# Kernel optimization log

Hardware: AMD Instinct MI355X
Metric: run time of the kernel (lower is better)

The kernel has to match this reference:

```python
import jax, jax.numpy as jnp
import numpy as np

N_EMBD = 1024
HEAD_SIZE = 64
B, T = 4, 4096


def setup_inputs() -> dict:
    key = jax.random.key(0)
    kx, kk, kq, kv = jax.random.split(key, 4)
    s = 1.0 / np.sqrt(N_EMBD)
    return {
        "x": jax.random.normal(kx, (B, T, N_EMBD), dtype=jnp.float32),
        "Wk": jax.random.normal(kk, (N_EMBD, HEAD_SIZE), dtype=jnp.float32) * s,
        "Wq": jax.random.normal(kq, (N_EMBD, HEAD_SIZE), dtype=jnp.float32) * s,
        "Wv": jax.random.normal(kv, (N_EMBD, HEAD_SIZE), dtype=jnp.float32) * s,
    }


def reference(x, Wk, Wq, Wv):
    Bb, Tt, C = x.shape
    k = x @ Wk  # [B,T,H]
    q = x @ Wq
    v = x @ Wv
    # scores scaled by C**-0.5 where C = n_embd (as in the original module)
    w = jnp.einsum('bth,bsh->bts', q, k) * (C ** -0.5)  # [B,T,T]
    causal = jnp.tril(jnp.ones((Tt, Tt), dtype=bool))
    w = jnp.where(causal, w, -jnp.inf)
    w = jax.nn.softmax(w, axis=-1)
    # dropout prob is 0.0 (eval) -> identity
    out = jnp.einsum('bts,bsh->bth', w, v)  # [B,T,H]
    return out
```

## Files before the change

### kernel.cpp

```cpp
#include <hip/hip_runtime.h>


#define BSZ 4
#define TSZ 4096
#define CSZ 1024
#define MSZ (BSZ * TSZ)
#define QT 128
#define NQT (TSZ / QT)
#define CPB 272
#define MAXC 16

typedef _Float16 half8 __attribute__((ext_vector_type(8)));
typedef _Float16 half4 __attribute__((ext_vector_type(4)));
typedef float f32x4 __attribute__((ext_vector_type(4)));

#define MFMA(a, b, c) __builtin_amdgcn_mfma_f32_16x16x32_f16((a), (b), (c), 0, 0, 0)
#define QSCALE 0.04508422002778011f

__device__ __forceinline__ int kimg(int r, int h) {
    return r * 64 + (((h >> 3) ^ (r & 7)) << 3) + (h & 7);
}
__device__ __forceinline__ int vimg(int kk, int h) {
    int p = (kk & 15) * 4 + (kk >> 4);
    return h * 64 + (((p >> 3) ^ (h & 7)) << 3) + (p & 7);
}

__device__ __forceinline__ void glds16(const _Float16* g, _Float16* l) {
    __builtin_amdgcn_global_load_lds(
        (const __attribute__((address_space(1))) void*)g,
        (__attribute__((address_space(3))) void*)l, 16, 0, 0);
}

__global__ __launch_bounds__(192) void wconv(const float* __restrict__ Wk,
                                             const float* __restrict__ Wq,
                                             const float* __restrict__ Wv,
                                             _Float16* __restrict__ Wt) {
    int k = blockIdx.x;
    int n = threadIdx.x;
    int g = k >> 6, c = (k >> 3) & 7, j = k & 7;
    const float* W = (n < 64) ? Wk : ((n < 128) ? Wq : Wv);
    float v = W[k * 64 + (n & 63)];
    if (n >= 64 && n < 128) v *= QSCALE;
    Wt[(size_t)n * 1024 + g * 64 + ((c ^ (n & 7)) << 3) + j] = (_Float16)v;
}

__global__ __launch_bounds__(512) void qkv_proj(
    const float* __restrict__ x, const _Float16* __restrict__ Wt,
    _Float16* __restrict__ qbf, _Float16* __restrict__ kvs) {
    __shared__ _Float16 wt[2][192 * 64];
    __shared__ _Float16 xt[2][64 * 64];

    int tid = threadIdx.x;
    int wave = tid >> 6, lane = tid & 63;
    int quad = lane >> 4, l16 = lane & 15;
    int row0 = blockIdx.x * 64;
    int mh = wave >> 2;
    int ctb = (wave & 3) * 3;

    f32x4 acc[6];
#pragma unroll
    for (int i = 0; i < 6; i++) acc[i] = (f32x4){0.f, 0.f, 0.f, 0.f};

    int sr = tid >> 3, sc = tid & 7;
    const float* xrow = x + (size_t)(row0 + sr) * CSZ + sc * 8;
    f32x4 p0 = *(const f32x4*)xrow;
    f32x4 p1 = *(const f32x4*)(xrow + 4);

#pragma unroll
    for (int i = 0; i < 3; i++) {
        int g = i * 512 + tid;
        glds16(Wt + ((size_t)(g >> 3)) * 1024 + (g & 7) * 8,
               &wt[0][(size_t)g * 8]);
    }

    int cur = 0;
    for (int kc = 0; kc < CSZ; kc += 64, cur ^= 1) {
        {
            _Float16 tmp[8] __attribute__((aligned(16)));
#pragma unroll
            for (int i = 0; i < 4; i++) {
                tmp[i] = (_Float16)p0[i];
                tmp[4 + i] = (_Float16)p1[i];
            }
            *(half8*)&xt[cur][sr * 64 + ((sc ^ (sr & 7)) << 3)] = *(half8*)tmp;
        }
        __syncthreads();

        if (kc + 64 < CSZ) {
#pragma unroll
            for (int i = 0; i < 3; i++) {
                int g = i * 512 + tid;
                glds16(Wt + ((size_t)(g >> 3)) * 1024 + (kc + 64) + (g & 7) * 8,
                       &wt[cur ^ 1][(size_t)g * 8]);
            }
            p0 = *(const f32x4*)(xrow + kc + 64);
            p1 = *(const f32x4*)(xrow + kc + 68);
        }

#pragma unroll
        for (int ss = 0; ss < 2; ss++) {
            half8 a0 = *(half8*)&xt[cur][(mh * 32 + l16) * 64 +
                                         (((ss * 4 + quad) ^ (l16 & 7)) << 3)];
            half8 a1 = *(half8*)&xt[cur][(mh * 32 + 16 + l16) * 64 +
                                         (((ss * 4 + quad) ^ (l16 & 7)) << 3)];
#pragma unroll
            for (int j = 0; j < 3; j++) {
                int ct = ctb + j;
                half8 bb = *(half8*)&wt[cur][(ct * 16 + l16) * 64 +
                                             (((ss * 4 + quad) ^ (l16 & 7))
                                              << 3)];
                acc[j * 2 + 0] = MFMA(a0, bb, acc[j * 2 + 0]);
                acc[j * 2 + 1] = MFMA(a1, bb, acc[j * 2 + 1]);
            }
        }
    }

#pragma unroll
    for (int j = 0; j < 3; j++) {
        int ct = ctb + j;
        int kind = ct >> 2;
        int col = (ct & 3) * 16 + l16;
#pragma unroll
        for (int m = 0; m < 2; m++) {
#pragma unroll
            for (int r = 0; r < 4; r++) {
                int row = row0 + mh * 32 + m * 16 + quad * 4 + r;
                _Float16 val = (_Float16)acc[j * 2 + m][r];
                if (kind == 0) {
                    kvs[((size_t)(row >> 6)) * 8192 + kimg(row & 63, col)] = val;
                } else if (kind == 1) {
                    qbf[(size_t)row * 64 + col] = val;
                } else {
                    kvs[((size_t)(row >> 6)) * 8192 + 4096 +
                        vimg(row & 63, col)] = val;
                }
            }
        }
    }
}

__global__ __launch_bounds__(256) void attn_partial(
    const _Float16* __restrict__ qbf, const _Float16* __restrict__ kvs,
    _Float16* __restrict__ opart, float* __restrict__ ml) {
    __shared__ _Float16 kt[2][4096];
    __shared__ _Float16 vt[2][4096];
    __shared__ _Float16 pt[QT * 64];

    int tid = threadIdx.x;
    int wave = tid >> 6, lane = tid & 63;
    int quad = lane >> 4, l16 = lane & 15;

    int id = blockIdx.x;
    int xcd = id & 7;
    int b = xcd >> 1;
    int id2 = (id >> 3) * 2 + (xcd & 1);
    int qt = 0;
    while (qt < NQT - 1 && (((qt + 2) * (qt + 2)) >> 2) <= id2) qt++;
    int chunk = id2 - (((qt + 1) * (qt + 1)) >> 2);
    int nt = 2 * (qt + 1);
    int lo = chunk * 4;
    int hi = min(lo + 4, nt);
    int part = (b * NQT + qt) * MAXC + chunk;

    const _Float16* qb = qbf + (size_t)b * TSZ * 64;
    const _Float16* kvb = kvs + (size_t)b * 64 * 8192;

    int qrow = qt * QT + wave * 32;
    half8 aq[2][2];
#pragma unroll
    for (int st = 0; st < 2; st++)
#pragma unroll
        for (int ss = 0; ss < 2; ss++)
            aq[st][ss] = *(const half8*)&qb[(size_t)(qrow + st * 16 + l16) * 64 +
                                            ss * 32 + quad * 8];

    f32x4 o[2][4];
    float l_acc[2][4];
#pragma unroll
    for (int st = 0; st < 2; st++)
#pragma unroll
        for (int ct = 0; ct < 4; ct++) {
            o[st][ct] = (f32x4){0.f, 0.f, 0.f, 0.f};
            l_acc[st][ct] = 0.f;
        }

    int soff = wave * 512 + lane * 8;

    {
        const _Float16* p0 = kvb + (size_t)lo * 8192 + soff;
        glds16(p0, &kt[0][soff]);
        glds16(p0 + 2048, &kt[0][2048 + soff]);
        glds16(p0 + 4096, &vt[0][soff]);
        glds16(p0 + 6144, &vt[0][2048 + soff]);
    }

    int cur = 0;
    for (int kti = lo; kti < hi; kti++, cur ^= 1) {
        __syncthreads();
        if (kti + 1 < hi) {
            const _Float16* p0 = kvb + (size_t)(kti + 1) * 8192 + soff;
            glds16(p0, &kt[cur ^ 1][soff]);
            glds16(p0 + 2048, &kt[cur ^ 1][2048 + soff]);
            glds16(p0 + 4096, &vt[cur ^ 1][soff]);
            glds16(p0 + 6144, &vt[cur ^ 1][2048 + soff]);
        }

        f32x4 sacc[2][4];
#pragma unroll
        for (int st = 0; st < 2; st++)
#pragma unroll
            for (int ct = 0; ct < 4; ct++)
                sacc[st][ct] = (f32x4){0.f, 0.f, 0.f, 0.f};
#pragma unroll
        for (int ss = 0; ss < 2; ss++) {
#pragma unroll
            for (int ct = 0; ct < 4; ct++) {
                half8 bb = *(half8*)&kt[cur][(ct * 16 + l16) * 64 +
                                             (((ss * 4 + quad) ^ (l16 & 7))
                                              << 3)];
                sacc[0][ct] = MFMA(aq[0][ss], bb, sacc[0][ct]);
                sacc[1][ct] = MFMA(aq[1][ss], bb, sacc[1][ct]);
            }
        }

        bool diag = (kti >= 2 * qt);
#pragma unroll
        for (int st = 0; st < 2; st++) {
#pragma unroll
            for (int r = 0; r < 4; r++) {
                int lrow = wave * 32 + st * 16 + quad * 4 + r;
                float pv[4];
#pragma unroll
                for (int ct = 0; ct < 4; ct++) {
                    float e = exp2f(sacc[st][ct][r]);
                    if (diag) {
                        int key = kti * 64 + ct * 16 + l16;
                        if (key > qt * QT + lrow) e = 0.f;
                    }
                    pv[ct] = e;
                }
                l_acc[st][r] += pv[0] + pv[1] + pv[2] + pv[3];
                half4 hp;
#pragma unroll
                for (int ct = 0; ct < 4; ct++) hp[ct] = (_Float16)pv[ct];
                int chk = (l16 >> 1) ^ (lrow & 7);
                *(half4*)&pt[lrow * 64 + chk * 8 + (l16 & 1) * 4] = hp;
            }
        }

#pragma unroll
        for (int ss = 0; ss < 2; ss++) {
            half8 ap0 = *(half8*)&pt[(wave * 32 + l16) * 64 +
                                     (((ss * 4 + quad) ^ (l16 & 7)) << 3)];
            half8 ap1 = *(half8*)&pt[(wave * 32 + 16 + l16) * 64 +
                                     (((ss * 4 + quad) ^ (l16 & 7)) << 3)];
#pragma unroll
            for (int ct = 0; ct < 4; ct++) {
                half8 bv = *(half8*)&vt[cur][(ct * 16 + l16) * 64 +
                                             (((ss * 4 + quad) ^ (l16 & 7))
                                              << 3)];
                o[0][ct] = MFMA(ap0, bv, o[0][ct]);
                o[1][ct] = MFMA(ap1, bv, o[1][ct]);
            }
        }
    }

#pragma unroll
    for (int off = 1; off < 16; off <<= 1) {
#pragma unroll
        for (int st = 0; st < 2; st++)
#pragma unroll
            for (int r = 0; r < 4; r++)
                l_acc[st][r] += __shfl_xor(l_acc[st][r], off);
    }

    _Float16* op = opart + (size_t)part * (QT * 64);
#pragma unroll
    for (int st = 0; st < 2; st++) {
#pragma unroll
        for (int r = 0; r < 4; r++) {
            int lrow = wave * 32 + st * 16 + quad * 4 + r;
            float li = l_acc[st][r];
            float inv = li > 0.f ? 1.f / li : 0.f;
#pragma unroll
            for (int ct = 0; ct < 4; ct++)
                op[lrow * 64 + ct * 16 + l16] = (_Float16)(o[st][ct][r] * inv);
            if (l16 == 0) ml[part * QT + lrow] = li;
        }
    }
}

__global__ __launch_bounds__(256) void combine(
    const _Float16* __restrict__ opart, const float* __restrict__ ml,
    float* __restrict__ out) {
    int tid = threadIdx.x;
    int row = blockIdx.x * 32 + (tid >> 3);
    int seg = (tid & 7) * 8;
    int b = row >> 12;
    int qt = (row >> 7) & (NQT - 1);
    int prow = row & (QT - 1);
    int pbase = (b * NQT + qt) * MAXC;
    int nc = (qt + 2) >> 1;

    float acc[8];
#pragma unroll
    for (int i = 0; i < 8; i++) acc[i] = 0.f;
    float lsum = 0.f;
    for (int s = 0; s < nc; s++) {
        float l = ml[(pbase + s) * QT + prow];
        lsum += l;
        half8 h = *(const half8*)&opart[(size_t)(pbase + s) * (QT * 64) +
                                        prow * 64 + seg];
#pragma unroll
        for (int i = 0; i < 8; i++) acc[i] += l * (float)h[i];
    }
    float inv = 1.f / lsum;
    float* ob = out + (size_t)row * 64 + seg;
#pragma unroll
    for (int i = 0; i < 8; i++) ob[i] = acc[i] * inv;
}

extern "C" void kernel_launch(void* const* d_in, const int* in_sizes, int n_in,
                              void* d_out, int out_size, void* d_ws,
                              size_t ws_size, hipStream_t stream) {
    (void)in_sizes; (void)n_in; (void)out_size; (void)ws_size;
    const float* x = (const float*)d_in[0];
    const float* Wk = (const float*)d_in[1];
    const float* Wq = (const float*)d_in[2];
    const float* Wv = (const float*)d_in[3];

    _Float16* Wt = (_Float16*)d_ws;
    _Float16* qbf = Wt + 192 * 1024;
    _Float16* kvs = qbf + (size_t)MSZ * 64;
    _Float16* opart = kvs + (size_t)MSZ * 128;
    float* ml = (float*)(opart + (size_t)BSZ * NQT * MAXC * QT * 64);

    wconv<<<1024, 192, 0, stream>>>(Wk, Wq, Wv, Wt);
    qkv_proj<<<MSZ / 64, 512, 0, stream>>>(x, Wt, qbf, kvs);
    attn_partial<<<BSZ * CPB, 256, 0, stream>>>(qbf, kvs, opart, ml);
    combine<<<MSZ / 32, 256, 0, stream>>>(opart, ml, (float*)d_out);
}
```

Baseline: 150.4 us.

## Use 32x32x16 MFMA with transposed S and register-resident P for PV

Rewrites the attention inner loop to compute S^T with 32x32x16 MFMAs so each lane owns one query row. P is packed to fp16 in registers and rearranged with permlane32 swaps, then fed straight into the PV MFMA, which removes the LDS round-trip through the P tile. The V storage layout changes to match, and fully masked 32-key subtiles on the diagonal are skipped. It also adds setprio around the MFMA groups and a min-4-blocks occupancy hint, at the cost of more complex lane mapping and inline asm.

```diff
diff --git a/kernel.cpp b/kernel.cpp
--- a/kernel.cpp
+++ b/kernel.cpp
@@ -13,16 +13,17 @@
 typedef _Float16 half8 __attribute__((ext_vector_type(8)));
 typedef _Float16 half4 __attribute__((ext_vector_type(4)));
 typedef float f32x4 __attribute__((ext_vector_type(4)));
+typedef float f32x16 __attribute__((ext_vector_type(16)));
 
 #define MFMA(a, b, c) __builtin_amdgcn_mfma_f32_16x16x32_f16((a), (b), (c), 0, 0, 0)
+#define MFMA32(a, b, c) __builtin_amdgcn_mfma_f32_32x32x16_f16((a), (b), (c), 0, 0, 0)
 #define QSCALE 0.04508422002778011f
 
 __device__ __forceinline__ int kimg(int r, int h) {
     return r * 64 + (((h >> 3) ^ (r & 7)) << 3) + (h & 7);
 }
 __device__ __forceinline__ int vimg(int kk, int h) {
-    int p = (kk & 15) * 4 + (kk >> 4);
-    return h * 64 + (((p >> 3) ^ (h & 7)) << 3) + (p & 7);
+    return h * 64 + (((kk >> 3) ^ (h & 7)) << 3) + (kk & 7);
 }
 
 __device__ __forceinline__ void glds16(const _Float16* g, _Float16* l) {
@@ -139,16 +140,16 @@
     }
 }
 
-__global__ __launch_bounds__(256) void attn_partial(
+__global__ __launch_bounds__(256, 4) void attn_partial(
     const _Float16* __restrict__ qbf, const _Float16* __restrict__ kvs,
     _Float16* __restrict__ opart, float* __restrict__ ml) {
     __shared__ _Float16 kt[2][4096];
     __shared__ _Float16 vt[2][4096];
-    __shared__ _Float16 pt[QT * 64];
+    __shared__ float ls[4][32];
 
     int tid = threadIdx.x;
     int wave = tid >> 6, lane = tid & 63;
-    int quad = lane >> 4, l16 = lane & 15;
+    int l32 = lane & 31, hi = lane >> 5;
 
     int id = blockIdx.x;
     int xcd = id & 7;
@@ -159,30 +160,22 @@
     int chunk = id2 - (((qt + 1) * (qt + 1)) >> 2);
     int nt = 2 * (qt + 1);
     int lo = chunk * 4;
-    int hi = min(lo + 4, nt);
+    int hic = min(lo + 4, nt);
     int part = (b * NQT + qt) * MAXC + chunk;
 
     const _Float16* qb = qbf + (size_t)b * TSZ * 64;
     const _Float16* kvb = kvs + (size_t)b * 64 * 8192;
 
-    int qrow = qt * QT + wave * 32;
-    half8 aq[2][2];
-#pragma unroll
-    for (int st = 0; st < 2; st++)
-#pragma unroll
-        for (int ss = 0; ss < 2; ss++)
-            aq[st][ss] = *(const half8*)&qb[(size_t)(qrow + st * 16 + l16) * 64 +
-                                            ss * 32 + quad * 8];
-
-    f32x4 o[2][4];
-    float l_acc[2][4];
-#pragma unroll
-    for (int st = 0; st < 2; st++)
-#pragma unroll
-        for (int ct = 0; ct < 4; ct++) {
-            o[st][ct] = (f32x4){0.f, 0.f, 0.f, 0.f};
-            l_acc[st][ct] = 0.f;
-        }
+    int qrow = qt * QT + wave * 32 + l32;
+    half8 aq[4];
+#pragma unroll
+    for (int ss = 0; ss < 4; ss++)
+        aq[ss] = *(const half8*)&qb[(size_t)qrow * 64 + ss * 16 + hi * 8];
+
+    f32x16 o[2];
+#pragma unroll
+    for (int i = 0; i < 16; i++) { o[0][i] = 0.f; o[1][i] = 0.f; }
+    float l_acc = 0.f;
 
     int soff = wave * 512 + lane * 8;
 
@@ -195,9 +188,9 @@
     }
 
     int cur = 0;
-    for (int kti = lo; kti < hi; kti++, cur ^= 1) {
+    for (int kti = lo; kti < hic; kti++, cur ^= 1) {
         __syncthreads();
-        if (kti + 1 < hi) {
+        if (kti + 1 < hic) {
             const _Float16* p0 = kvb + (size_t)(kti + 1) * 8192 + soff;
             glds16(p0, &kt[cur ^ 1][soff]);
             glds16(p0 + 2048, &kt[cur ^ 1][2048 + soff]);
@@ -205,89 +198,81 @@
             glds16(p0 + 6144, &vt[cur ^ 1][2048 + soff]);
         }
 
-        f32x4 sacc[2][4];
-#pragma unroll
-        for (int st = 0; st < 2; st++)
-#pragma unroll
-            for (int ct = 0; ct < 4; ct++)
-                sacc[st][ct] = (f32x4){0.f, 0.f, 0.f, 0.f};
-#pragma unroll
-        for (int ss = 0; ss < 2; ss++) {
-#pragma unroll
-            for (int ct = 0; ct < 4; ct++) {
-                half8 bb = *(half8*)&kt[cur][(ct * 16 + l16) * 64 +
-                                             (((ss * 4 + quad) ^ (l16 & 7))
-                                              << 3)];
-                sacc[0][ct] = MFMA(aq[0][ss], bb, sacc[0][ct]);
-                sacc[1][ct] = MFMA(aq[1][ss], bb, sacc[1][ct]);
-            }
-        }
-
         bool diag = (kti >= 2 * qt);
-#pragma unroll
-        for (int st = 0; st < 2; st++) {
-#pragma unroll
-            for (int r = 0; r < 4; r++) {
-                int lrow = wave * 32 + st * 16 + quad * 4 + r;
-                float pv[4];
-#pragma unroll
-                for (int ct = 0; ct < 4; ct++) {
-                    float e = exp2f(sacc[st][ct][r]);
-                    if (diag) {
-                        int key = kti * 64 + ct * 16 + l16;
-                        if (key > qt * QT + lrow) e = 0.f;
-                    }
-                    pv[ct] = e;
+        int qrel = qrow - kti * 64;
+        int wmax = qt * QT + wave * 32 + 31 - kti * 64;
+
+#pragma unroll
+        for (int ctk = 0; ctk < 2; ctk++) {
+            if (diag && ctk * 32 > wmax) continue;
+
+            f32x16 s;
+#pragma unroll
+            for (int i = 0; i < 16; i++) s[i] = 0.f;
+            __builtin_amdgcn_s_setprio(1);
+#pragma unroll
+            for (int ss = 0; ss < 4; ss++) {
+                half8 ak = *(half8*)&kt[cur][kimg(ctk * 32 + l32,
+                                                  ss * 16 + hi * 8)];
+                s = MFMA32(ak, aq[ss], s);
+            }
+            __builtin_amdgcn_s_setprio(0);
+
+            float e[16];
+#pragma unroll
+            for (int r = 0; r < 16; r++) {
+                float ev = exp2f(s[r]);
+                if (diag) {
+                    int key = ctk * 32 + (r & 3) + 8 * (r >> 2) + 4 * hi;
+                    if (key > qrel) ev = 0.f;
                 }
-                l_acc[st][r] += pv[0] + pv[1] + pv[2] + pv[3];
-                half4 hp;
-#pragma unroll
-                for (int ct = 0; ct < 4; ct++) hp[ct] = (_Float16)pv[ct];
-                int chk = (l16 >> 1) ^ (lrow & 7);
-                *(half4*)&pt[lrow * 64 + chk * 8 + (l16 & 1) * 4] = hp;
-            }
-        }
-
-#pragma unroll
-        for (int ss = 0; ss < 2; ss++) {
-            half8 ap0 = *(half8*)&pt[(wave * 32 + l16) * 64 +
-                                     (((ss * 4 + quad) ^ (l16 & 7)) << 3)];
-            half8 ap1 = *(half8*)&pt[(wave * 32 + 16 + l16) * 64 +
-                                     (((ss * 4 + quad) ^ (l16 & 7)) << 3)];
-#pragma unroll
-            for (int ct = 0; ct < 4; ct++) {
-                half8 bv = *(half8*)&vt[cur][(ct * 16 + l16) * 64 +
-                                             (((ss * 4 + quad) ^ (l16 & 7))
-                                              << 3)];
-                o[0][ct] = MFMA(ap0, bv, o[0][ct]);
-                o[1][ct] = MFMA(ap1, bv, o[1][ct]);
-            }
-        }
-    }
-
-#pragma unroll
-    for (int off = 1; off < 16; off <<= 1) {
-#pragma unroll
-        for (int st = 0; st < 2; st++)
-#pragma unroll
-            for (int r = 0; r < 4; r++)
-                l_acc[st][r] += __shfl_xor(l_acc[st][r], off);
-    }
+                e[r] = ev;
+                l_acc += ev;
+            }
+
+            unsigned pk[8];
+#pragma unroll
+            for (int p = 0; p < 8; p++) {
+                auto h2 = __builtin_amdgcn_cvt_pkrtz(e[2 * p], e[2 * p + 1]);
+                union { decltype(h2) h; unsigned u; } cv;
+                cv.h = h2;
+                pk[p] = cv.u;
+            }
+            asm("v_permlane32_swap_b32 %0, %1" : "+v"(pk[0]), "+v"(pk[2]));
+            asm("v_permlane32_swap_b32 %0, %1" : "+v"(pk[1]), "+v"(pk[3]));
+            asm("v_permlane32_swap_b32 %0, %1" : "+v"(pk[4]), "+v"(pk[6]));
+            asm("v_permlane32_swap_b32 %0, %1" : "+v"(pk[5]), "+v"(pk[7]));
+            union { unsigned u[4]; half8 h; } A0, A1;
+            A0.u[0] = pk[0]; A0.u[1] = pk[1]; A0.u[2] = pk[2]; A0.u[3] = pk[3];
+            A1.u[0] = pk[4]; A1.u[1] = pk[5]; A1.u[2] = pk[6]; A1.u[3] = pk[7];
+
+            __builtin_amdgcn_s_setprio(1);
+#pragma unroll
+            for (int cth = 0; cth < 2; cth++) {
+                int h = cth * 32 + l32;
+                half8 v0 = *(half8*)&vt[cur][vimg((2 * ctk + 0) * 16 + hi * 8, h)];
+                half8 v1 = *(half8*)&vt[cur][vimg((2 * ctk + 1) * 16 + hi * 8, h)];
+                o[cth] = MFMA32(A0.h, v0, o[cth]);
+                o[cth] = MFMA32(A1.h, v1, o[cth]);
+            }
+            __builtin_amdgcn_s_setprio(0);
+        }
+    }
+
+    l_acc += __shfl_xor(l_acc, 32);
+    float inv = l_acc > 0.f ? 1.f / l_acc : 0.f;
+    if (!hi) ls[wave][l32] = inv;
 
     _Float16* op = opart + (size_t)part * (QT * 64);
 #pragma unroll
-    for (int st = 0; st < 2; st++) {
-#pragma unroll
-        for (int r = 0; r < 4; r++) {
-            int lrow = wave * 32 + st * 16 + quad * 4 + r;
-            float li = l_acc[st][r];
-            float inv = li > 0.f ? 1.f / li : 0.f;
-#pragma unroll
-            for (int ct = 0; ct < 4; ct++)
-                op[lrow * 64 + ct * 16 + l16] = (_Float16)(o[st][ct][r] * inv);
-            if (l16 == 0) ml[part * QT + lrow] = li;
-        }
-    }
+    for (int r = 0; r < 16; r++) {
+        int rl = (r & 3) + 8 * (r >> 2) + 4 * hi;
+        float invr = ls[wave][rl];
+        int lrow = wave * 32 + rl;
+        op[lrow * 64 + l32] = (_Float16)(o[0][r] * invr);
+        op[lrow * 64 + 32 + l32] = (_Float16)(o[1][r] * invr);
+    }
+    if (!hi) ml[part * QT + wave * 32 + l32] = l_acc;
 }
 
 __global__ __launch_bounds__(256) void combine(
```

Result: faster. 143.9 us (-4.3%).
